# Optimization experiments

Measured on AMD Instinct MI355X. Metric: run time of the kernel, lower is better.

Reference implementation:

```python
import jax, jax.numpy as jnp
import numpy as np

N, E, K, F, R = 100000, 200000, 16, 32, 2
EPS = 1e-5

def setup_inputs() -> dict:
    key = jax.random.key(0)
    ks = jax.random.split(key, 32)
    inp = {}
    inp['x'] = jax.random.normal(ks[0], (N, F), jnp.float32)
    inp['y'] = jax.random.normal(ks[1], (E, F), jnp.float32)
    inp['deg_g'] = jax.random.uniform(ks[2], (N, 1), jnp.float32)
    inp['deg_lg'] = jax.random.uniform(ks[3], (E, 1), jnp.float32)
    inp['t_g'] = jax.random.randint(ks[4], (N, K), 0, N)
    inp['tt_g'] = jax.random.randint(ks[5], (N, K), 0, N)
    inp['t_lg'] = jax.random.randint(ks[6], (E, K), 0, E)
    inp['tt_lg'] = jax.random.randint(ks[7], (E, K), 0, E)
    inp['dst'] = jax.random.randint(ks[8], (E,), 0, N)
    inp['pm_pd'] = jax.random.randint(ks[9], (E,), 0, N)
    i = [10]
    def mk(shape):
        a = jax.random.normal(ks[i[0]], shape, jnp.float32) * 0.1
        i[0] += 1
        return a
    for nm in ['theta_x', 'theta_deg', 'theta_y', 'gamma_y', 'gamma_deg', 'gamma_x']:
        inp[nm + '_w'] = mk((F, F)); inp[nm + '_b'] = mk((F,))
    inp['theta_r_w'] = mk((R, F, F)); inp['theta_r_b'] = mk((R, F))
    inp['gamma_r_w'] = mk((R, F, F)); inp['gamma_r_b'] = mk((R, F))
    inp['bn_x_w'] = jnp.ones((F,), jnp.float32); inp['bn_x_b'] = jnp.zeros((F,), jnp.float32)
    inp['bn_y_w'] = jnp.ones((F,), jnp.float32); inp['bn_y_b'] = jnp.zeros((F,), jnp.float32)
    return inp

def _lin(a, w, b):
    return a @ w + b

def _bn(a, w, b):
    # BatchNorm1d in training mode: biased batch stats
    m = a.mean(axis=0)
    v = a.var(axis=0)
    return (a - m) / jnp.sqrt(v + EPS) * w + b

def _aggregate(z, t, tt):
    # per-node gather+sum over neighbor index lists (t: radius-0, tt: radius-1)
    return jnp.stack([z[t].sum(axis=1), z[tt].sum(axis=1)])  # [R, M, F]

def reference(x, y, deg_g, deg_lg, t_g, tt_g, t_lg, tt_lg, dst, pm_pd,
              theta_x_w, theta_x_b, theta_deg_w, theta_deg_b, theta_y_w, theta_y_b,
              gamma_y_w, gamma_y_b, gamma_deg_w, gamma_deg_b, gamma_x_w, gamma_x_b,
              theta_r_w, theta_r_b, gamma_r_w, gamma_r_b,
              bn_x_w, bn_x_b, bn_y_w, bn_y_b):
    n = F // 2
    pmpd_x = x[pm_pd]                                   # [E, F] embedding gather
    zs = _aggregate(x, t_g, tt_g)                        # [R, N, F]
    sum_x = jnp.einsum('rnf,rfo->no', zs, theta_r_w) + theta_r_b.sum(axis=0)
    pmpd_y = jax.ops.segment_sum(y, dst, num_segments=x.shape[0])  # copy_edge + sum
    xo = (_lin(x, theta_x_w, theta_x_b)
          + _lin(deg_g * x, theta_deg_w, theta_deg_b)
          + sum_x
          + _lin(pmpd_y, theta_y_w, theta_y_b))
    xo = jnp.concatenate([xo[:, :n], jax.nn.relu(xo[:, n:])], axis=1)
    xo = _bn(xo, bn_x_w, bn_x_b)
    zy = _aggregate(y, t_lg, tt_lg)                      # [R, E, F]
    sum_y = jnp.einsum('ref,rfo->eo', zy, gamma_r_w) + gamma_r_b.sum(axis=0)
    yo = (_lin(y, gamma_y_w, gamma_y_b)
          + _lin(deg_lg * y, gamma_deg_w, gamma_deg_b)
          + sum_y
          + _lin(pmpd_x, gamma_x_w, gamma_x_b))
    yo = jnp.concatenate([yo[:, :n], jax.nn.relu(yo[:, n:])], axis=1)
    yo = _bn(yo, bn_y_w, bn_y_b)
    return xo, yo
```

## Files before the change

### kernel.cpp

```cpp
#include <hip/hip_runtime.h>

#define NN 100000
#define NE 200000
#define MT (NN + NE)

typedef unsigned short u16;
typedef __attribute__((ext_vector_type(8))) short bf16x8;
typedef __attribute__((ext_vector_type(4))) float f32x4;

__device__ __forceinline__ float bf2f(u16 u) {
    union { unsigned int i; float f; } v; v.i = ((unsigned int)u) << 16; return v.f;
}
__device__ __forceinline__ u16 f2bf(float f) {
    union { unsigned int i; float f; } v; v.f = f;
    unsigned int r = v.i + 0x7fffu + ((v.i >> 16) & 1u);
    return (u16)(r >> 16);
}
__device__ __forceinline__ void unpack2(unsigned int u, float& lo, float& hi) {
    union { unsigned int i; float f; } a, b;
    a.i = u << 16; b.i = u & 0xffff0000u;
    lo = a.f; hi = b.f;
}
__device__ __forceinline__ unsigned int pack2(float a, float b) {
    return (unsigned int)f2bf(a) | ((unsigned int)f2bf(b) << 16);
}
__device__ __forceinline__ float loadf(const void* p, size_t i, int f32) {
    return f32 ? ((const float*)p)[i] : bf2f(((const u16*)p)[i]);
}

__global__ void detect_kernel(const unsigned int* __restrict__ x, int* flag) {
    __shared__ int cnt;
    if (threadIdx.x == 0) cnt = 0;
    __syncthreads();
    int bad = 0;
    for (int i = threadIdx.x; i < 1024; i += 256) {
        unsigned int e = (x[i] >> 7) & 0xFF;
        if (e == 0xFF || (e > 0 && (e < 107 || e > 134))) bad++;
    }
    atomicAdd(&cnt, bad);
    __syncthreads();
    if (threadIdx.x == 0) *flag = (cnt > 256) ? 1 : 0;
}

__global__ __launch_bounds__(256) void prep_kernel(
    const void* txw, const void* tdw, const void* tyw,
    const void* gyw, const void* gdw, const void* gxw,
    const void* trw, const void* grw,
    const void* txb, const void* tdb, const void* tyb,
    const void* gyb, const void* gdb, const void* gxb,
    const void* trb, const void* grb,
    u16* Bfx, u16* Bfy, float* bx, float* by, const int* flagp)
{
    int f32 = *flagp;
    int t = blockIdx.x * 256 + threadIdx.x;
    if (t < 10240) {
        int side = t / 5120;
        int e = t - side * 5120;
        int b = e >> 9, lane = (e >> 3) & 63, j = e & 7;
        int m = b >> 1;
        int k = ((lane >> 4) << 3) + j;
        int f = ((b & 1) << 4) + (lane & 15);
        size_t idx = (size_t)k * 32 + f;
        float v;
        if (side == 0) {
            v = (m == 0) ? loadf(txw, idx, f32) : (m == 1) ? loadf(tdw, idx, f32)
              : (m == 2) ? loadf(trw, idx, f32) : (m == 3) ? loadf(trw, 1024 + idx, f32)
              : loadf(gxw, idx, f32);
            Bfx[e] = f2bf(v);
        } else {
            v = (m == 0) ? loadf(gyw, idx, f32) : (m == 1) ? loadf(gdw, idx, f32)
              : (m == 2) ? loadf(grw, idx, f32) : (m == 3) ? loadf(grw, 1024 + idx, f32)
              : loadf(tyw, idx, f32);
            Bfy[e] = f2bf(v);
        }
    } else if (t < 10304) {
        int f = t - 10240;
        if (f < 32) {
            bx[f] = loadf(txb, f, f32) + loadf(tdb, f, f32) + loadf(tyb, f, f32)
                  + loadf(trb, f, f32) + loadf(trb, 32 + f, f32);
        } else {
            f -= 32;
            by[f] = loadf(gyb, f, f32) + loadf(gdb, f, f32) + loadf(gxb, f, f32)
                  + loadf(grb, f, f32) + loadf(grb, 32 + f, f32);
        }
    }
}

__global__ __launch_bounds__(256, 4) void gemm2(
    const void* __restrict__ x, const void* __restrict__ y,
    const u16* __restrict__ Bfx, const u16* __restrict__ Bfy,
    const float* __restrict__ bx, const float* __restrict__ by,
    const void* __restrict__ deg_g, const void* __restrict__ deg_lg,
    const int* __restrict__ dst,
    u16* __restrict__ Xself, u16* __restrict__ Xt,
    u16* __restrict__ Xtt,   u16* __restrict__ Xaux,
    u16* __restrict__ Yself, u16* __restrict__ Yt, u16* __restrict__ Ytt,
    float* __restrict__ xacc, const int* __restrict__ flagp)
{
    int f32 = *flagp;
    int lane = threadIdx.x & 63;
    int wib  = threadIdx.x >> 6;
    bool is_y = (blockIdx.x >= 1563);
    int wid = (is_y ? (int)blockIdx.x - 1563 : (int)blockIdx.x) * 4 + wib;
    int nwaves = is_y ? 12500 : 6250;
    if (wid >= nwaves) return;
    int r0 = wid * 16;

    const void* feat = is_y ? y : x;
    const u16* Bf   = is_y ? Bfy : Bfx;
    const float* bias = is_y ? by : bx;
    const void* deg  = is_y ? deg_lg : deg_g;

    union { u16 s[8]; bf16x8 v; } au;
    {
        size_t eoff = (size_t)(r0 + (lane & 15)) * 32 + ((lane >> 4) << 3);
        if (f32) {
            const float4* fp = (const float4*)((const float*)feat + eoff);
            float4 A0 = fp[0], A1 = fp[1];
            au.s[0] = f2bf(A0.x); au.s[1] = f2bf(A0.y);
            au.s[2] = f2bf(A0.z); au.s[3] = f2bf(A0.w);
            au.s[4] = f2bf(A1.x); au.s[5] = f2bf(A1.y);
            au.s[6] = f2bf(A1.z); au.s[7] = f2bf(A1.w);
        } else {
            au.v = *(const bf16x8*)((const u16*)feat + eoff);
        }
    }
    f32x4 acc[10];
    const u16* bp = Bf + lane * 8;
#pragma unroll
    for (int b = 0; b < 10; ++b) {
        bf16x8 bfr = *(const bf16x8*)(bp + b * 512);
        f32x4 z = {0.f, 0.f, 0.f, 0.f};
        acc[b] = __builtin_amdgcn_mfma_f32_16x16x32_bf16(au.v, bfr, z, 0, 0, 0);
    }

    int n = lane & 15, quad = lane >> 4;
    int rowb = r0 + quad * 4;
    float bl = bias[n], bh = bias[16 + n];

#pragma unroll
    for (int i = 0; i < 4; ++i) {
        float dgi = loadf(deg, rowb + i, f32);
        size_t ro = (size_t)(rowb + i) * 32;
        u16 s_lo = f2bf(acc[0][i] + dgi * acc[2][i] + bl);
        u16 s_hi = f2bf(acc[1][i] + dgi * acc[3][i] + bh);
        if (!is_y) {
            Xself[ro + n]      = s_lo;
            Xself[ro + 16 + n] = s_hi;
            Xt[ro + n]         = f2bf(acc[4][i]);
            Xt[ro + 16 + n]    = f2bf(acc[5][i]);
            Xtt[ro + n]        = f2bf(acc[6][i]);
            Xtt[ro + 16 + n]   = f2bf(acc[7][i]);
            Xaux[ro + n]       = f2bf(acc[8][i]);
            Xaux[ro + 16 + n]  = f2bf(acc[9][i]);
        } else {
            Yself[ro + n]      = s_lo;
            Yself[ro + 16 + n] = s_hi;
            Yt[ro + n]         = f2bf(acc[4][i]);
            Yt[ro + 16 + n]    = f2bf(acc[5][i]);
            Ytt[ro + n]        = f2bf(acc[6][i]);
            Ytt[ro + 16 + n]   = f2bf(acc[7][i]);
            int d = dst[rowb + i];
            float* p = xacc + (size_t)d * 32;
            atomicAdd(p + n,      acc[8][i]);
            atomicAdd(p + 16 + n, acc[9][i]);
        }
    }
}

__global__ __launch_bounds__(256) void gather_fused(
    const u16* __restrict__ Xself, const u16* __restrict__ Xt,
    const u16* __restrict__ Xtt,   const u16* __restrict__ Xaux,
    const u16* __restrict__ Yself, const u16* __restrict__ Yt,
    const u16* __restrict__ Ytt,
    const float* __restrict__ xacc,
    const int* __restrict__ t_g, const int* __restrict__ tt_g,
    const int* __restrict__ t_lg, const int* __restrict__ tt_lg,
    const int* __restrict__ pm_pd,
    float* __restrict__ xpre, u16* __restrict__ ypre,
    float* __restrict__ stats)
{
    __shared__ int s_t[1024];
    __shared__ int s_tt[1024];
    __shared__ float s_sum[32];
    __shared__ float s_sq[32];
    bool is_y = (blockIdx.x >= 1563);
    int M = is_y ? NE : NN;
    const u16 *Self, *T, *TT;
    const int *tl, *ttl;
    if (is_y) { Self = Yself; T = Yt; TT = Ytt; tl = t_lg; ttl = tt_lg; }
    else      { Self = Xself; T = Xt; TT = Xtt; tl = t_g;  ttl = tt_g; }
    float* ss = stats + (is_y ? 64 : 0);

    if (threadIdx.x < 32) { s_sum[threadIdx.x] = 0.f; s_sq[threadIdx.x] = 0.f; }
    int row0 = (is_y ? (int)blockIdx.x - 1563 : (int)blockIdx.x) * 64;
    int lim = (M - row0) * 16;
    for (int i = threadIdx.x; i < 1024; i += 256) {
        s_t[i]  = (i < lim) ? tl[row0 * 16 + i]  : 0;
        s_tt[i] = (i < lim) ? ttl[row0 * 16 + i] : 0;
    }
    __syncthreads();

    int lr = threadIdx.x >> 2, q = threadIdx.x & 3;
    int r = row0 + lr;
    bool act = r < M;
    int rc = act ? r : row0;

    float a[8];
    {
        uint4 u = *(const uint4*)(Self + (size_t)rc * 32 + q * 8);
        unpack2(u.x, a[0], a[1]); unpack2(u.y, a[2], a[3]);
        unpack2(u.z, a[4], a[5]); unpack2(u.w, a[6], a[7]);
    }
    const int* il = &s_t[lr * 16];
    const int* ill = &s_tt[lr * 16];
#pragma unroll
    for (int batch = 0; batch < 2; ++batch) {
        uint4 g[8];
#pragma unroll
        for (int j = 0; j < 8; ++j)
            g[j] = *(const uint4*)(T + (size_t)il[batch * 8 + j] * 32 + q * 8);
#pragma unroll
        for (int j = 0; j < 8; ++j) {
            float e0, e1, e2, e3, e4, e5, e6, e7;
            unpack2(g[j].x, e0, e1); unpack2(g[j].y, e2, e3);
            unpack2(g[j].z, e4, e5); unpack2(g[j].w, e6, e7);
            a[0] += e0; a[1] += e1; a[2] += e2; a[3] += e3;
            a[4] += e4; a[5] += e5; a[6] += e6; a[7] += e7;
        }
    }
#pragma unroll
    for (int batch = 0; batch < 2; ++batch) {
        uint4 g[8];
#pragma unroll
        for (int j = 0; j < 8; ++j)
            g[j] = *(const uint4*)(TT + (size_t)ill[batch * 8 + j] * 32 + q * 8);
#pragma unroll
        for (int j = 0; j < 8; ++j) {
            float e0, e1, e2, e3, e4, e5, e6, e7;
            unpack2(g[j].x, e0, e1); unpack2(g[j].y, e2, e3);
            unpack2(g[j].z, e4, e5); unpack2(g[j].w, e6, e7);
            a[0] += e0; a[1] += e1; a[2] += e2; a[3] += e3;
            a[4] += e4; a[5] += e5; a[6] += e6; a[7] += e7;
        }
    }
    if (!is_y) {
        float4 b0 = *(const float4*)(xacc + (size_t)rc * 32 + q * 8);
        float4 b1 = *(const float4*)(xacc + (size_t)rc * 32 + q * 8 + 4);
        a[0] += b0.x; a[1] += b0.y; a[2] += b0.z; a[3] += b0.w;
        a[4] += b1.x; a[5] += b1.y; a[6] += b1.z; a[7] += b1.w;
    } else {
        int ai = pm_pd[rc];
        uint4 g = *(const uint4*)(Xaux + (size_t)ai * 32 + q * 8);
        float e0, e1, e2, e3, e4, e5, e6, e7;
        unpack2(g.x, e0, e1); unpack2(g.y, e2, e3);
        unpack2(g.z, e4, e5); unpack2(g.w, e6, e7);
        a[0] += e0; a[1] += e1; a[2] += e2; a[3] += e3;
        a[4] += e4; a[5] += e5; a[6] += e6; a[7] += e7;
    }
    if (q >= 2) {
#pragma unroll
        for (int i = 0; i < 8; ++i) a[i] = fmaxf(a[i], 0.f);
    }
    if (act) {
        if (!is_y) {
            float4 o0, o1;
            o0.x = a[0]; o0.y = a[1]; o0.z = a[2]; o0.w = a[3];
            o1.x = a[4]; o1.y = a[5]; o1.z = a[6]; o1.w = a[7];
            *(float4*)(xpre + (size_t)r * 32 + q * 8) = o0;
            *(float4*)(xpre + (size_t)r * 32 + q * 8 + 4) = o1;
        } else {
            uint4 o;
            o.x = pack2(a[0], a[1]); o.y = pack2(a[2], a[3]);
            o.z = pack2(a[4], a[5]); o.w = pack2(a[6], a[7]);
            *(uint4*)(ypre + (size_t)r * 32 + q * 8) = o;
        }
    } else {
#pragma unroll
        for (int i = 0; i < 8; ++i) a[i] = 0.f;
    }
#pragma unroll
    for (int i = 0; i < 8; ++i) {
        atomicAdd(&s_sum[q * 8 + i], a[i]);
        atomicAdd(&s_sq[q * 8 + i], a[i] * a[i]);
    }
    __syncthreads();
    if (threadIdx.x < 32) {
        atomicAdd(&ss[threadIdx.x], s_sum[threadIdx.x]);
        atomicAdd(&ss[32 + threadIdx.x], s_sq[threadIdx.x]);
    }
}

__global__ void finalize_stats(
    const float* stats,
    const void* bnxw, const void* bnxb, const void* bnyw, const void* bnyb,
    float* scsh, const int* flagp)
{
    int f32 = *flagp;
    int f = threadIdx.x;
    if (f < 32) {
        float m = stats[f] / (float)NN;
        float var = stats[32 + f] / (float)NN - m * m;
        float inv = rsqrtf(var + 1e-5f);
        float sc = loadf(bnxw, f, f32) * inv;
        scsh[f] = sc; scsh[32 + f] = loadf(bnxb, f, f32) - m * sc;
    } else if (f < 64) {
        int g = f - 32;
        float m = stats[64 + g] / (float)NE;
        float var = stats[96 + g] / (float)NE - m * m;
        float inv = rsqrtf(var + 1e-5f);
        float sc = loadf(bnyw, g, f32) * inv;
        scsh[64 + g] = sc; scsh[96 + g] = loadf(bnyb, g, f32) - m * sc;
    }
}

__global__ __launch_bounds__(256) void apply_bn(
    const float* __restrict__ xpre, const u16* __restrict__ ypre,
    const float* __restrict__ scsh, void* __restrict__ out,
    const int* __restrict__ flagp)
{
    int f32 = *flagp;
    int tid = blockIdx.x * 256 + threadIdx.x;
    if (tid >= MT * 8) return;
    int fq = (tid & 7) * 4;
    const float* sc;
    float4 v;
    if (tid < NN * 8) {
        v = ((const float4*)xpre)[tid];
        sc = scsh;
    } else {
        size_t off = (size_t)tid * 4 - (size_t)NN * 32;
        ushort4 u = *(const ushort4*)(ypre + off);
        v.x = bf2f(u.x); v.y = bf2f(u.y); v.z = bf2f(u.z); v.w = bf2f(u.w);
        sc = scsh + 64;
    }
    float o0 = v.x * sc[fq + 0] + sc[32 + fq + 0];
    float o1 = v.y * sc[fq + 1] + sc[32 + fq + 1];
    float o2 = v.z * sc[fq + 2] + sc[32 + fq + 2];
    float o3 = v.w * sc[fq + 3] + sc[32 + fq + 3];
    if (f32) {
        float4 o; o.x = o0; o.y = o1; o.z = o2; o.w = o3;
        ((float4*)out)[tid] = o;
    } else {
        ushort4 o; o.x = f2bf(o0); o.y = f2bf(o1); o.z = f2bf(o2); o.w = f2bf(o3);
        ((ushort4*)out)[tid] = o;
    }
}

extern "C" void kernel_launch(void* const* d_in, const int* in_sizes, int n_in,
                              void* d_out, int out_size, void* d_ws, size_t ws_size,
                              hipStream_t stream)
{
    const void* x      = d_in[0];
    const void* y      = d_in[1];
    const void* deg_g  = d_in[2];
    const void* deg_lg = d_in[3];
    const int* t_g   = (const int*)d_in[4];
    const int* tt_g  = (const int*)d_in[5];
    const int* t_lg  = (const int*)d_in[6];
    const int* tt_lg = (const int*)d_in[7];
    const int* dst   = (const int*)d_in[8];
    const int* pm_pd = (const int*)d_in[9];

    char* ws = (char*)d_ws;
    int*   flag = (int*)ws;
    u16* Bfx   = (u16*)(ws + 256);
    u16* Bfy   = Bfx + 5120;
    float* bx  = (float*)(ws + 24576);
    float* by  = bx + 32;
    float* stats = by + 32;
    float* scsh  = stats + 128;
    u16* Xself = (u16*)(ws + 65536);
    u16* Xt    = Xself + (size_t)NN * 32;
    u16* Xtt   = Xt    + (size_t)NN * 32;
    u16* Xaux  = Xtt   + (size_t)NN * 32;
    u16* Yself = Xaux  + (size_t)NN * 32;
    u16* Yt    = Yself + (size_t)NE * 32;
    u16* Ytt   = Yt    + (size_t)NE * 32;
    float* xacc = (float*)(Ytt + (size_t)NE * 32);
    u16* ypre = (u16*)(xacc + (size_t)NN * 32);

    hipMemsetAsync(stats, 0, 256 * sizeof(float), stream);
    hipMemsetAsync(xacc, 0, (size_t)NN * 32 * sizeof(float), stream);

    detect_kernel<<<1, 256, 0, stream>>>((const unsigned int*)x, flag);
    prep_kernel<<<41, 256, 0, stream>>>(
        d_in[10], d_in[12], d_in[14], d_in[16], d_in[18], d_in[20],
        d_in[22], d_in[24],
        d_in[11], d_in[13], d_in[15], d_in[17], d_in[19], d_in[21],
        d_in[23], d_in[25],
        Bfx, Bfy, bx, by, flag);
    gemm2<<<4688, 256, 0, stream>>>(x, y, Bfx, Bfy, bx, by, deg_g, deg_lg, dst,
                                    Xself, Xt, Xtt, Xaux, Yself, Yt, Ytt,
                                    xacc, flag);
    gather_fused<<<4688, 256, 0, stream>>>(Xself, Xt, Xtt, Xaux, Yself, Yt, Ytt,
                                           xacc, t_g, tt_g, t_lg, tt_lg, pm_pd,
                                           xacc, ypre, stats);
    finalize_stats<<<1, 64, 0, stream>>>(stats, d_in[26], d_in[27], d_in[28],
                                         d_in[29], scsh, flag);
    apply_bn<<<9375, 256, 0, stream>>>(xacc, ypre, scsh, d_out, flag);
}
```

Measured before the change: 424.2 us.

## Stage GEMM outputs through LDS for coalesced stores and unify bf16 pre-BN buffer

The weight fragments are permuted so each lane's MFMA output columns are adjacent feature pairs. Results are packed into LDS per wave, then written to global memory as 16-byte coalesced rows instead of scattered 2-byte stores. The x-side pre-BN output now goes to a single bf16 buffer instead of fp32, which shrinks gather and apply_bn traffic at some precision cost. The gather loop is rebatched into 4x4 loads and given a 6-block occupancy hint, trading per-thread memory-level parallelism for more resident waves.

```diff
diff --git a/kernel.cpp b/kernel.cpp
--- a/kernel.cpp
+++ b/kernel.cpp
@@ -5,36 +5,37 @@
 #define MT (NN + NE)
 
 typedef unsigned short u16;
+typedef unsigned int u32;
 typedef __attribute__((ext_vector_type(8))) short bf16x8;
 typedef __attribute__((ext_vector_type(4))) float f32x4;
 
 __device__ __forceinline__ float bf2f(u16 u) {
-    union { unsigned int i; float f; } v; v.i = ((unsigned int)u) << 16; return v.f;
+    union { u32 i; float f; } v; v.i = ((u32)u) << 16; return v.f;
 }
 __device__ __forceinline__ u16 f2bf(float f) {
-    union { unsigned int i; float f; } v; v.f = f;
-    unsigned int r = v.i + 0x7fffu + ((v.i >> 16) & 1u);
+    union { u32 i; float f; } v; v.f = f;
+    u32 r = v.i + 0x7fffu + ((v.i >> 16) & 1u);
     return (u16)(r >> 16);
 }
-__device__ __forceinline__ void unpack2(unsigned int u, float& lo, float& hi) {
-    union { unsigned int i; float f; } a, b;
+__device__ __forceinline__ void unpack2(u32 u, float& lo, float& hi) {
+    union { u32 i; float f; } a, b;
     a.i = u << 16; b.i = u & 0xffff0000u;
     lo = a.f; hi = b.f;
 }
-__device__ __forceinline__ unsigned int pack2(float a, float b) {
-    return (unsigned int)f2bf(a) | ((unsigned int)f2bf(b) << 16);
+__device__ __forceinline__ u32 pack2(float a, float b) {
+    return (u32)f2bf(a) | ((u32)f2bf(b) << 16);
 }
 __device__ __forceinline__ float loadf(const void* p, size_t i, int f32) {
     return f32 ? ((const float*)p)[i] : bf2f(((const u16*)p)[i]);
 }
 
-__global__ void detect_kernel(const unsigned int* __restrict__ x, int* flag) {
+__global__ void detect_kernel(const u32* __restrict__ x, int* flag) {
     __shared__ int cnt;
     if (threadIdx.x == 0) cnt = 0;
     __syncthreads();
     int bad = 0;
     for (int i = threadIdx.x; i < 1024; i += 256) {
-        unsigned int e = (x[i] >> 7) & 0xFF;
+        u32 e = (x[i] >> 7) & 0xFF;
         if (e == 0xFF || (e > 0 && (e < 107 || e > 134))) bad++;
     }
     atomicAdd(&cnt, bad);
@@ -59,7 +60,7 @@
         int b = e >> 9, lane = (e >> 3) & 63, j = e & 7;
         int m = b >> 1;
         int k = ((lane >> 4) << 3) + j;
-        int f = ((b & 1) << 4) + (lane & 15);
+        int f = ((lane & 15) << 1) | (b & 1);
         size_t idx = (size_t)k * 32 + f;
         float v;
         if (side == 0) {
@@ -97,6 +98,7 @@
     u16* __restrict__ Yself, u16* __restrict__ Yt, u16* __restrict__ Ytt,
     float* __restrict__ xacc, const int* __restrict__ flagp)
 {
+    __shared__ __align__(16) u16 sbuf[4][4][512];
     int f32 = *flagp;
     int lane = threadIdx.x & 63;
     int wib  = threadIdx.x >> 6;
@@ -136,39 +138,44 @@
 
     int n = lane & 15, quad = lane >> 4;
     int rowb = r0 + quad * 4;
-    float bl = bias[n], bh = bias[16 + n];
+    float bev = bias[2 * n], bov = bias[2 * n + 1];
 
 #pragma unroll
     for (int i = 0; i < 4; ++i) {
         float dgi = loadf(deg, rowb + i, f32);
-        size_t ro = (size_t)(rowb + i) * 32;
-        u16 s_lo = f2bf(acc[0][i] + dgi * acc[2][i] + bl);
-        u16 s_hi = f2bf(acc[1][i] + dgi * acc[3][i] + bh);
-        if (!is_y) {
-            Xself[ro + n]      = s_lo;
-            Xself[ro + 16 + n] = s_hi;
-            Xt[ro + n]         = f2bf(acc[4][i]);
-            Xt[ro + 16 + n]    = f2bf(acc[5][i]);
-            Xtt[ro + n]        = f2bf(acc[6][i]);
-            Xtt[ro + 16 + n]   = f2bf(acc[7][i]);
-            Xaux[ro + n]       = f2bf(acc[8][i]);
-            Xaux[ro + 16 + n]  = f2bf(acc[9][i]);
-        } else {
-            Yself[ro + n]      = s_lo;
-            Yself[ro + 16 + n] = s_hi;
-            Yt[ro + n]         = f2bf(acc[4][i]);
-            Yt[ro + 16 + n]    = f2bf(acc[5][i]);
-            Ytt[ro + n]        = f2bf(acc[6][i]);
-            Ytt[ro + 16 + n]   = f2bf(acc[7][i]);
+        int rr = (quad * 4 + i) * 32 + 2 * n;
+        *(u32*)&sbuf[wib][0][rr] = pack2(acc[0][i] + dgi * acc[2][i] + bev,
+                                         acc[1][i] + dgi * acc[3][i] + bov);
+        *(u32*)&sbuf[wib][1][rr] = pack2(acc[4][i], acc[5][i]);
+        *(u32*)&sbuf[wib][2][rr] = pack2(acc[6][i], acc[7][i]);
+        if (!is_y)
+            *(u32*)&sbuf[wib][3][rr] = pack2(acc[8][i], acc[9][i]);
+    }
+    __asm__ volatile("s_waitcnt lgkmcnt(0)" ::: "memory");
+
+    int lr = lane >> 2, ch = (lane & 3) * 8;
+    int lo = lr * 32 + ch;
+    size_t go = (size_t)(r0 + lr) * 32 + ch;
+    if (!is_y) {
+        *(uint4*)(Xself + go) = *(const uint4*)&sbuf[wib][0][lo];
+        *(uint4*)(Xt   + go)  = *(const uint4*)&sbuf[wib][1][lo];
+        *(uint4*)(Xtt  + go)  = *(const uint4*)&sbuf[wib][2][lo];
+        *(uint4*)(Xaux + go)  = *(const uint4*)&sbuf[wib][3][lo];
+    } else {
+        *(uint4*)(Yself + go) = *(const uint4*)&sbuf[wib][0][lo];
+        *(uint4*)(Yt   + go)  = *(const uint4*)&sbuf[wib][1][lo];
+        *(uint4*)(Ytt  + go)  = *(const uint4*)&sbuf[wib][2][lo];
+#pragma unroll
+        for (int i = 0; i < 4; ++i) {
             int d = dst[rowb + i];
             float* p = xacc + (size_t)d * 32;
-            atomicAdd(p + n,      acc[8][i]);
-            atomicAdd(p + 16 + n, acc[9][i]);
-        }
-    }
-}
-
-__global__ __launch_bounds__(256) void gather_fused(
+            atomicAdd(p + 2 * n,     acc[8][i]);
+            atomicAdd(p + 2 * n + 1, acc[9][i]);
+        }
+    }
+}
+
+__global__ __launch_bounds__(256, 6) void gather_fused(
     const u16* __restrict__ Xself, const u16* __restrict__ Xt,
     const u16* __restrict__ Xtt,   const u16* __restrict__ Xaux,
     const u16* __restrict__ Yself, const u16* __restrict__ Yt,
@@ -177,7 +184,7 @@
     const int* __restrict__ t_g, const int* __restrict__ tt_g,
     const int* __restrict__ t_lg, const int* __restrict__ tt_lg,
     const int* __restrict__ pm_pd,
-    float* __restrict__ xpre, u16* __restrict__ ypre,
+    u16* __restrict__ pre_h,
     float* __restrict__ stats)
 {
     __shared__ int s_t[1024];
@@ -212,16 +219,16 @@
         unpack2(u.x, a[0], a[1]); unpack2(u.y, a[2], a[3]);
         unpack2(u.z, a[4], a[5]); unpack2(u.w, a[6], a[7]);
     }
-    const int* il = &s_t[lr * 16];
+    const int* il  = &s_t[lr * 16];
     const int* ill = &s_tt[lr * 16];
 #pragma unroll
-    for (int batch = 0; batch < 2; ++batch) {
-        uint4 g[8];
-#pragma unroll
-        for (int j = 0; j < 8; ++j)
-            g[j] = *(const uint4*)(T + (size_t)il[batch * 8 + j] * 32 + q * 8);
-#pragma unroll
-        for (int j = 0; j < 8; ++j) {
+    for (int batch = 0; batch < 4; ++batch) {
+        uint4 g[4];
+#pragma unroll
+        for (int j = 0; j < 4; ++j)
+            g[j] = *(const uint4*)(T + (size_t)il[batch * 4 + j] * 32 + q * 8);
+#pragma unroll
+        for (int j = 0; j < 4; ++j) {
             float e0, e1, e2, e3, e4, e5, e6, e7;
             unpack2(g[j].x, e0, e1); unpack2(g[j].y, e2, e3);
             unpack2(g[j].z, e4, e5); unpack2(g[j].w, e6, e7);
@@ -230,13 +237,13 @@
         }
     }
 #pragma unroll
-    for (int batch = 0; batch < 2; ++batch) {
-        uint4 g[8];
-#pragma unroll
-        for (int j = 0; j < 8; ++j)
-            g[j] = *(const uint4*)(TT + (size_t)ill[batch * 8 + j] * 32 + q * 8);
-#pragma unroll
-        for (int j = 0; j < 8; ++j) {
+    for (int batch = 0; batch < 4; ++batch) {
+        uint4 g[4];
+#pragma unroll
+        for (int j = 0; j < 4; ++j)
+            g[j] = *(const uint4*)(TT + (size_t)ill[batch * 4 + j] * 32 + q * 8);
+#pragma unroll
+        for (int j = 0; j < 4; ++j) {
             float e0, e1, e2, e3, e4, e5, e6, e7;
             unpack2(g[j].x, e0, e1); unpack2(g[j].y, e2, e3);
             unpack2(g[j].z, e4, e5); unpack2(g[j].w, e6, e7);
@@ -263,18 +270,11 @@
         for (int i = 0; i < 8; ++i) a[i] = fmaxf(a[i], 0.f);
     }
     if (act) {
-        if (!is_y) {
-            float4 o0, o1;
-            o0.x = a[0]; o0.y = a[1]; o0.z = a[2]; o0.w = a[3];
-            o1.x = a[4]; o1.y = a[5]; o1.z = a[6]; o1.w = a[7];
-            *(float4*)(xpre + (size_t)r * 32 + q * 8) = o0;
-            *(float4*)(xpre + (size_t)r * 32 + q * 8 + 4) = o1;
-        } else {
-            uint4 o;
-            o.x = pack2(a[0], a[1]); o.y = pack2(a[2], a[3]);
-            o.z = pack2(a[4], a[5]); o.w = pack2(a[6], a[7]);
-            *(uint4*)(ypre + (size_t)r * 32 + q * 8) = o;
-        }
+        size_t orow = (size_t)(is_y ? NN + r : r) * 32 + q * 8;
+        uint4 o;
+        o.x = pack2(a[0], a[1]); o.y = pack2(a[2], a[3]);
+        o.z = pack2(a[4], a[5]); o.w = pack2(a[6], a[7]);
+        *(uint4*)(pre_h + orow) = o;
     } else {
 #pragma unroll
         for (int i = 0; i < 8; ++i) a[i] = 0.f;
@@ -315,29 +315,19 @@
 }
 
 __global__ __launch_bounds__(256) void apply_bn(
-    const float* __restrict__ xpre, const u16* __restrict__ ypre,
-    const float* __restrict__ scsh, void* __restrict__ out,
-    const int* __restrict__ flagp)
+    const u16* __restrict__ pre_h, const float* __restrict__ scsh,
+    void* __restrict__ out, const int* __restrict__ flagp)
 {
     int f32 = *flagp;
     int tid = blockIdx.x * 256 + threadIdx.x;
     if (tid >= MT * 8) return;
     int fq = (tid & 7) * 4;
-    const float* sc;
-    float4 v;
-    if (tid < NN * 8) {
-        v = ((const float4*)xpre)[tid];
-        sc = scsh;
-    } else {
-        size_t off = (size_t)tid * 4 - (size_t)NN * 32;
-        ushort4 u = *(const ushort4*)(ypre + off);
-        v.x = bf2f(u.x); v.y = bf2f(u.y); v.z = bf2f(u.z); v.w = bf2f(u.w);
-        sc = scsh + 64;
-    }
-    float o0 = v.x * sc[fq + 0] + sc[32 + fq + 0];
-    float o1 = v.y * sc[fq + 1] + sc[32 + fq + 1];
-    float o2 = v.z * sc[fq + 2] + sc[32 + fq + 2];
-    float o3 = v.w * sc[fq + 3] + sc[32 + fq + 3];
+    const float* sc = (tid < NN * 8) ? scsh : scsh + 64;
+    ushort4 u = ((const ushort4*)pre_h)[tid];
+    float o0 = bf2f(u.x) * sc[fq + 0] + sc[32 + fq + 0];
+    float o1 = bf2f(u.y) * sc[fq + 1] + sc[32 + fq + 1];
+    float o2 = bf2f(u.z) * sc[fq + 2] + sc[32 + fq + 2];
+    float o3 = bf2f(u.w) * sc[fq + 3] + sc[32 + fq + 3];
     if (f32) {
         float4 o; o.x = o0; o.y = o1; o.z = o2; o.w = o3;
         ((float4*)out)[tid] = o;
@@ -378,12 +368,12 @@
     u16* Yt    = Yself + (size_t)NE * 32;
     u16* Ytt   = Yt    + (size_t)NE * 32;
     float* xacc = (float*)(Ytt + (size_t)NE * 32);
-    u16* ypre = (u16*)(xacc + (size_t)NN * 32);
+    u16* pre_h = (u16*)(xacc + (size_t)NN * 32);
 
     hipMemsetAsync(stats, 0, 256 * sizeof(float), stream);
     hipMemsetAsync(xacc, 0, (size_t)NN * 32 * sizeof(float), stream);
 
-    detect_kernel<<<1, 256, 0, stream>>>((const unsigned int*)x, flag);
+    detect_kernel<<<1, 256, 0, stream>>>((const u32*)x, flag);
     prep_kernel<<<41, 256, 0, stream>>>(
         d_in[10], d_in[12], d_in[14], d_in[16], d_in[18], d_in[20],
         d_in[22], d_in[24],
@@ -395,8 +385,8 @@
                                     xacc, flag);
     gather_fused<<<4688, 256, 0, stream>>>(Xself, Xt, Xtt, Xaux, Yself, Yt, Ytt,
                                            xacc, t_g, tt_g, t_lg, tt_lg, pm_pd,
-                                           xacc, ypre, stats);
+                                           pre_h, stats);
     finalize_stats<<<1, 64, 0, stream>>>(stats, d_in[26], d_in[27], d_in[28],
                                          d_in[29], scsh, flag);
-    apply_bn<<<9375, 256, 0, stream>>>(xacc, ypre, scsh, d_out, flag);
-}
+    apply_bn<<<9375, 256, 0, stream>>>(pre_h, scsh, d_out, flag);
+}
```

Result: slower. 646.5 us (+52.4%).
